# Performance work log

Measured on AMD Instinct MI355X. Metric: run time of the kernel, lower is better.

Reference implementation:

```python
import jax, jax.numpy as jnp
import numpy as np

EPS_BN = 1e-5
EPS_LN = 1e-5

def _bn(x, g, b, m, v):
    # inference-mode BatchNorm2d over channel dim 1
    scale = g / jnp.sqrt(v + EPS_BN)
    return x * scale[None, :, None, None] + (b - m * scale)[None, :, None, None]

def _conv1x1(x, w, b=None):
    y = jnp.einsum('bchw,oc->bohw', x, w)
    if b is not None:
        y = y + b[None, :, None, None]
    return y

def _gelu(x):
    return jax.nn.gelu(x, approximate=False)

def setup_inputs() -> dict:
    key = jax.random.key(0)
    ks = jax.random.split(key, 40)
    B, C, H, W = 32, 160, 56, 56
    C5, C3 = C // 5, C * 3
    s = 0.05
    d = {}
    d['x'] = jax.random.normal(ks[0], (B, C, H, W), jnp.float32)
    d['bn1_g'] = jax.random.uniform(ks[1], (C,), jnp.float32, 0.5, 1.5)
    d['bn1_b'] = jax.random.normal(ks[2], (C,)) * s
    d['bn1_m'] = jax.random.normal(ks[3], (C,)) * s
    d['bn1_v'] = jnp.ones((C,), jnp.float32)
    names = ['t', 'b', 'r', 'l', 'c']
    for i, n in enumerate(names):
        d['w' + n] = jax.random.normal(ks[4 + i], (C5, C)) * s
        d['b' + n] = jax.random.normal(ks[9 + i], (C5,)) * s
    d['wf1'] = jax.random.normal(ks[14], (C, C)) * s
    d['bf1'] = jax.random.normal(ks[15], (C,)) * s
    d['bn2_g'] = jax.random.uniform(ks[16], (C,), jnp.float32, 0.5, 1.5)
    d['bn2_b'] = jax.random.normal(ks[17], (C,)) * s
    d['bn2_m'] = jax.random.normal(ks[18], (C,)) * s
    d['bn2_v'] = jnp.ones((C,), jnp.float32)
    d['wph'] = jax.random.normal(ks[19], (W, W)) * s
    d['bph'] = jax.random.normal(ks[20], (W,)) * s
    d['wpw'] = jax.random.normal(ks[21], (H, H)) * s
    d['bpw'] = jax.random.normal(ks[22], (H,)) * s
    d['wf2'] = jax.random.normal(ks[23], (C, C3)) * s
    d['ln_g'] = jax.random.uniform(ks[24], (C,), jnp.float32, 0.5, 1.5)
    d['ln_b'] = jax.random.normal(ks[25], (C,)) * s
    d['wfc1'] = jax.random.normal(ks[26], (C3, C)) * s
    d['bfc1'] = jax.random.normal(ks[27], (C3,)) * s
    d['wfc2'] = jax.random.normal(ks[28], (C, C3)) * s
    d['bfc2'] = jax.random.normal(ks[29], (C,)) * s
    d['step'] = 1
    return d

def reference(x, bn1_g, bn1_b, bn1_m, bn1_v, wt, bt, wb, bb, wr, br, wl, bl, wc, bc,
              wf1, bf1, bn2_g, bn2_b, bn2_m, bn2_v, wph, bph, wpw, bpw, wf2,
              ln_g, ln_b, wfc1, bfc1, wfc2, bfc2, step):
    B, C, H, W = x.shape
    # ---- localMix: ShiftedPillarsConcatentation_BNAct_NP5 ----
    h = _gelu(_bn(x, bn1_g, bn1_b, bn1_m, bn1_v))
    x_t = _conv1x1(h, wt, bt)
    x_b = _conv1x1(h, wb, bb)
    x_r = _conv1x1(h, wr, br)
    x_l = _conv1x1(h, wl, bl)
    x_c = _conv1x1(h, wc, bc)
    # pad then narrow exactly as torch: t/l shift by 1, b/r shift by step
    x_t = jnp.pad(x_t, ((0, 0), (0, 0), (0, step), (0, 0)))[:, :, 1:1 + H, :]
    x_b = jnp.pad(x_b, ((0, 0), (0, 0), (step, 0), (0, 0)))[:, :, 0:H, :]
    x_l = jnp.pad(x_l, ((0, 0), (0, 0), (0, 0), (0, step)))[:, :, :, 1:1 + W]
    x_r = jnp.pad(x_r, ((0, 0), (0, 0), (0, 0), (step, 0)))[:, :, :, 0:W]
    lm = _conv1x1(jnp.concatenate([x_t, x_b, x_r, x_l, x_c], axis=1), wf1, bf1)
    # ---- globalMix: sparseMLP_BNAct ----
    g = _gelu(_bn(lm, bn2_g, bn2_b, bn2_m, bn2_v))
    # proj_h mixes the W axis (input permuted to (B,W,C,H)), bias per output W
    x_h = jnp.einsum('bchw,vw->bchv', g, wph) + bph[None, None, None, :]
    # proj_w mixes the H axis (input permuted to (B,H,C,W)), bias per output H
    x_w = jnp.einsum('bchw,uh->bcuw', g, wpw) + bpw[None, None, :, None]
    gm = _conv1x1(jnp.concatenate([g, x_h, x_w], axis=1), wf2)  # no bias
    x1 = gm + x  # residual 1
    # ---- channelMix: LN + Mlp over channels ----
    y = jnp.transpose(x1, (0, 2, 3, 1))  # BHWC
    mu = jnp.mean(y, axis=-1, keepdims=True)
    var = jnp.mean(jnp.square(y - mu), axis=-1, keepdims=True)
    y = (y - mu) / jnp.sqrt(var + EPS_LN) * ln_g + ln_b
    y = _gelu(jnp.einsum('bhwc,fc->bhwf', y, wfc1) + bfc1)
    y = jnp.einsum('bhwf,cf->bhwc', y, wfc2) + bfc2
    return jnp.transpose(y, (0, 3, 1, 2)) + x1  # residual 2
```

## Files before the change

kernel.cpp:

```cpp
#include <hip/hip_runtime.h>
#include <hip/hip_bf16.h>
#include <math.h>

typedef __hip_bfloat16 bf16;
typedef __attribute__((ext_vector_type(8))) short s8v;
typedef __attribute__((ext_vector_type(4))) float f4v;
typedef __attribute__((ext_vector_type(4))) unsigned short u4v;

#define Bn  32
#define Cn  160
#define HWn 3136
#define Pn  100352

__device__ __forceinline__ float b2f(bf16 v){ return __bfloat162float(v); }
__device__ __forceinline__ bf16  f2b(float v){ return __float2bfloat16(v); }
__device__ __forceinline__ float bits2f(unsigned short u){
    union { float f; unsigned int i; } x; x.i = ((unsigned int)u) << 16; return x.f;
}
__device__ __forceinline__ unsigned short f2bits(float v){
    union { unsigned short us; bf16 b; } cv; cv.b = f2b(v); return cv.us;
}
__device__ __forceinline__ float gelu_f(float x){
    float ax = fabsf(x) * 0.7071067811865476f;
    float t  = 1.0f / (1.0f + 0.3275911f*ax);
    float p  = ((((1.061405429f*t - 1.453152027f)*t + 1.421413741f)*t
                 - 0.284496736f)*t + 0.254829592f)*t;
    float e  = __expf(-ax*ax);
    float erfv = 1.0f - p*e;
    float s = (x >= 0.f) ? erfv : -erfv;
    return 0.5f*x*(1.0f + s);
}

#define MFMA(a,b,c) __builtin_amdgcn_mfma_f32_16x16x32_bf16((a),(b),(c),0,0,0)

__global__ __launch_bounds__(256) void k0_prep(
    const float* __restrict__ wt, const float* __restrict__ wb_, const float* __restrict__ wr,
    const float* __restrict__ wl, const float* __restrict__ wc,
    const float* __restrict__ bt, const float* __restrict__ bb_, const float* __restrict__ br,
    const float* __restrict__ bl, const float* __restrict__ bc,
    const float* __restrict__ wf1, const float* __restrict__ bf1,
    const float* __restrict__ g2, const float* __restrict__ b2, const float* __restrict__ m2, const float* __restrict__ v2,
    const float* __restrict__ wf2, const float* __restrict__ wfc1, const float* __restrict__ wfc2,
    const float* __restrict__ wph, const float* __restrict__ wpw,
    const float* __restrict__ lng, const float* __restrict__ lnb, const float* __restrict__ bfc1,
    bf16* wcat, bf16* wf1b, bf16* wf2b, bf16* wfc1g, bf16* wfc2b, bf16* wphb, bf16* wpwb,
    float* bcat, float* epsv, float* eptv, float* wgs, float* wcb)
{
    int idx = blockIdx.x*256 + threadIdx.x;
    if (idx < 25600){ int o = idx/160, k = idx - o*160; int gi = o>>5, oo = o&31;
        const float* wp = gi==0?wt: gi==1?wb_: gi==2?wr: gi==3?wl: wc;
        wcat[idx] = f2b(wp[oo*160+k]); return; }
    idx -= 25600;
    if (idx < 25600){ wf1b[idx] = f2b(wf1[idx]); return; }
    idx -= 25600;
    if (idx < 76800){ wf2b[idx] = f2b(wf2[idx]); return; }
    idx -= 76800;
    if (idx < 76800){ int f = idx/160, c = idx - f*160;
        wfc1g[idx] = f2b(wfc1[f*160+c] * lng[c]); return; }
    idx -= 76800;
    if (idx < 76800){ wfc2b[idx] = f2b(wfc2[idx]); return; }
    idx -= 76800;
    if (idx < 4096){ int v = idx>>6, w = idx&63;
        wphb[idx] = (v<56 && w<56) ? f2b(wph[v*56+w]) : f2b(0.f); return; }
    idx -= 4096;
    if (idx < 4096){ int v = idx>>6, w = idx&63;
        wpwb[idx] = (v<56 && w<56) ? f2b(wpw[v*56+w]) : f2b(0.f); return; }
    idx -= 4096;
    if (idx < 160){ int o = idx; int gi = o>>5, oo = o&31;
        const float* bp = gi==0?bt: gi==1?bb_: gi==2?br: gi==3?bl: bc;
        bcat[o] = bp[oo]; return; }
    idx -= 160;
    if (idx < 160){ int o = idx; float s = g2[o]*rsqrtf(v2[o]+1e-5f);
        epsv[o] = s; eptv[o] = (bf1[o]-m2[o])*s + b2[o]; return; }
    idx -= 160;
    if (idx < 480){ int o = idx; float sg = 0.f, sb = 0.f;
        const float* wr_ = wfc1 + (size_t)o*160;
        for (int c = 0; c < 160; ++c){ float w = wr_[c]; sg += w*lng[c]; sb += w*lnb[c]; }
        wgs[o] = sg; wcb[o] = sb + bfc1[o]; return; }
}

__global__ __launch_bounds__(256) void k12_bn_conv5(const float* __restrict__ x,
    const float* __restrict__ g, const float* __restrict__ b,
    const float* __restrict__ m_, const float* __restrict__ v,
    const bf16* __restrict__ wcat, const float* __restrict__ bcat, bf16* __restrict__ y5T)
{
    __shared__ __align__(16) unsigned short Bs[2][16*168];
    __shared__ __align__(16) char AsB[64*320];
    __shared__ float sc[160], sh[160];
    int tid = threadIdx.x, wave = tid>>6, lane = tid&63, m = lane&15, q = lane>>4;
    int blk = blockIdx.x; int bb = blk/49; int hw0 = (blk - bb*49)*64;
    if (tid < 160){
        float s = g[tid] * rsqrtf(v[tid] + 1e-5f);
        sc[tid] = s; sh[tid] = b[tid] - m_[tid]*s;
    }
    { const s8v* sp = (const s8v*)((const unsigned short*)wcat);
      for (int c = tid; c < 320; c += 256){ int row = c/20, col = (c - row*20)*8;
          *(s8v*)&Bs[0][row*168 + col] = sp[c]; } }
    __syncthreads();
    const float* xb = x + (size_t)bb*Cn*HWn + hw0;
    for (int idx = tid; idx < 160*64; idx += 256){
        int c = idx >> 6, p = idx & 63;
        float val = xb[(size_t)c*HWn + p];
        unsigned short us = f2bits(gelu_f(val*sc[c] + sh[c]));
        int off = (p*320 + c*2) ^ ((p&7)<<4);
        *(unsigned short*)(AsB + off) = us;
    }
    __syncthreads();
    size_t pos0 = (size_t)bb*HWn + hw0;
    s8v a[5];
    {
        int row = wave*16 + m; int xr = (row&7)<<4;
        #pragma unroll
        for (int kb = 0; kb < 5; ++kb){
            int off = (row*320 + (q*8 + kb*32)*2) ^ xr;
            a[kb] = *(const s8v*)(AsB + off);
        }
    }
    for (int s = 0; s < 10; ++s){
        if (s+1 < 10){
            const s8v* sp = (const s8v*)((const unsigned short*)wcat + (size_t)(s+1)*2560);
            for (int c = tid; c < 320; c += 256){ int row = c/20, col = (c - row*20)*8;
                *(s8v*)&Bs[(s+1)&1][row*168 + col] = sp[c]; }
        }
        f4v acc = {0.f,0.f,0.f,0.f};
        const unsigned short* Bp = &Bs[s&1][m*168 + q*8];
        #pragma unroll
        for (int kb = 0; kb < 5; ++kb) acc = MFMA(a[kb], *(const s8v*)(Bp + kb*32), acc);
        float bias = bcat[s*16 + m];
        bf16* yo = y5T + (pos0 + wave*16 + q*4)*160 + s*16 + m;
        #pragma unroll
        for (int r = 0; r < 4; ++r) yo[r*160] = f2b(acc[r] + bias);
        __syncthreads();
    }
}

__global__ __launch_bounds__(256) void k3_wf1(const bf16* __restrict__ y5T,
    const bf16* __restrict__ wf1b, const float* __restrict__ epsv, const float* __restrict__ eptv,
    bf16* __restrict__ gT)
{
    __shared__ __align__(16) unsigned short Bs[2][16*168];
    int tid = threadIdx.x, wave = tid>>6, lane = tid&63, m = lane&15, q = lane>>4;
    int blk = blockIdx.x; int bb = blk/49; int hw0 = (blk - bb*49)*64;
    size_t pos0 = (size_t)bb*HWn + hw0;
    int phw = hw0 + wave*16 + m; int h = phw/56, w = phw - h*56;
    s8v a[5];
    #pragma unroll
    for (int kb = 0; kb < 5; ++kb){
        int h2 = h, w2 = w; bool ok = true;
        if      (kb == 0){ h2 = h+1; ok = (h2 < 56); }
        else if (kb == 1){ h2 = h-1; ok = (h2 >= 0); }
        else if (kb == 2){ w2 = w-1; ok = (w2 >= 0); }
        else if (kb == 3){ w2 = w+1; ok = (w2 < 56); }
        if (ok){
            const unsigned short* Ap = (const unsigned short*)y5T +
                ((size_t)bb*HWn + h2*56 + w2)*160 + kb*32 + q*8;
            a[kb] = *(const s8v*)Ap;
        } else {
            a[kb] = (s8v){0,0,0,0,0,0,0,0};
        }
    }
    { const s8v* sp = (const s8v*)((const unsigned short*)wf1b);
      for (int c = tid; c < 320; c += 256){ int row = c/20, col = (c - row*20)*8;
          *(s8v*)&Bs[0][row*168 + col] = sp[c]; } }
    __syncthreads();
    for (int s = 0; s < 10; ++s){
        if (s+1 < 10){
            const s8v* sp = (const s8v*)((const unsigned short*)wf1b + (size_t)(s+1)*2560);
            for (int c = tid; c < 320; c += 256){ int row = c/20, col = (c - row*20)*8;
                *(s8v*)&Bs[(s+1)&1][row*168 + col] = sp[c]; }
        }
        f4v acc = {0.f,0.f,0.f,0.f};
        const unsigned short* Bp = &Bs[s&1][m*168 + q*8];
        #pragma unroll
        for (int kb = 0; kb < 5; ++kb) acc = MFMA(a[kb], *(const s8v*)(Bp + kb*32), acc);
        int o = s*16 + m;
        float es = epsv[o], et = eptv[o];
        bf16* go = gT + (pos0 + wave*16 + q*4)*160 + o;
        #pragma unroll
        for (int r = 0; r < 4; ++r) go[r*160] = f2b(gelu_f(acc[r]*es + et));
        __syncthreads();
    }
}

__global__ __launch_bounds__(256) void k4_projh(const bf16* __restrict__ gT,
    const bf16* __restrict__ wphb, const float* __restrict__ bph, bf16* __restrict__ xhT)
{
    __shared__ __align__(16) unsigned short gS[160*72];
    int tid = threadIdx.x, wave = tid>>6, lane = tid&63, m = lane&15, q = lane>>4;
    int blk = blockIdx.x; int b = blk/56, h = blk - b*56;
    const unsigned short* ga = (const unsigned short*)gT + ((size_t)b*HWn + h*56)*160;
    for (int idx = tid; idx < 56*160; idx += 256){
        int w = idx/160, c = idx - w*160;
        gS[c*72 + w] = ga[idx];
    }
    for (int idx = tid; idx < 160*8; idx += 256){
        int c = idx>>3, w = 56 + (idx&7);
        gS[c*72 + w] = 0;
    }
    __syncthreads();
    int v0 = wave*16;
    s8v a[2];
    #pragma unroll
    for (int kb = 0; kb < 2; ++kb)
        a[kb] = *(const s8v*)((const unsigned short*)wphb + (v0+m)*64 + kb*32 + q*8);
    int v = v0 + q*4;
    for (int s = 0; s < 10; ++s){
        f4v acc = {0.f,0.f,0.f,0.f};
        const unsigned short* Bp = &gS[(s*16+m)*72 + q*8];
        #pragma unroll
        for (int kb = 0; kb < 2; ++kb) acc = MFMA(a[kb], *(const s8v*)(Bp + kb*32), acc);
        #pragma unroll
        for (int r = 0; r < 4; ++r){
            int vv = v + r;
            if (vv < 56)
                xhT[((size_t)b*HWn + h*56 + vv)*160 + s*16 + m] = f2b(acc[r] + bph[vv]);
        }
    }
}

__global__ __launch_bounds__(256) void k5_projw(const bf16* __restrict__ gT,
    const bf16* __restrict__ wpwb, const float* __restrict__ bpw, bf16* __restrict__ xwT)
{
    __shared__ __align__(16) unsigned short gS[160*72];
    int tid = threadIdx.x, wave = tid>>6, lane = tid&63, m = lane&15, q = lane>>4;
    int blk = blockIdx.x; int b = blk/56, w = blk - b*56;
    const unsigned short* gbase = (const unsigned short*)gT + ((size_t)b*HWn + w)*160;
    for (int idx = tid; idx < 56*160; idx += 256){
        int hh = idx/160, c = idx - hh*160;
        gS[c*72 + hh] = gbase[(size_t)hh*56*160 + c];
    }
    for (int idx = tid; idx < 160*8; idx += 256){
        int c = idx>>3, hh = 56 + (idx&7);
        gS[c*72 + hh] = 0;
    }
    __syncthreads();
    int v0 = wave*16;
    s8v a[2];
    #pragma unroll
    for (int kb = 0; kb < 2; ++kb)
        a[kb] = *(const s8v*)((const unsigned short*)wpwb + (v0+m)*64 + kb*32 + q*8);
    int v = v0 + q*4;
    for (int s = 0; s < 10; ++s){
        f4v acc = {0.f,0.f,0.f,0.f};
        const unsigned short* Bp = &gS[(s*16+m)*72 + q*8];
        #pragma unroll
        for (int kb = 0; kb < 2; ++kb) acc = MFMA(a[kb], *(const s8v*)(Bp + kb*32), acc);
        #pragma unroll
        for (int r = 0; r < 4; ++r){
            int vv = v + r;
            if (vv < 56)
                xwT[((size_t)b*HWn + vv*56 + w)*160 + s*16 + m] = f2b(acc[r] + bpw[vv]);
        }
    }
}

__global__ __launch_bounds__(256) void k6_wf2(const bf16* __restrict__ gT,
    const bf16* __restrict__ xhT, const bf16* __restrict__ xwT,
    const bf16* __restrict__ wf2b, bf16* __restrict__ gm)
{
    __shared__ __align__(16) unsigned short Bs[2][16*488];
    int tid = threadIdx.x, wave = tid>>6, lane = tid&63, m = lane&15, q = lane>>4;
    size_t pos0 = (size_t)blockIdx.x*64;
    size_t prow = (pos0 + wave*16 + m)*160;
    s8v a[15];
    #pragma unroll
    for (int kb = 0; kb < 15; ++kb){
        const bf16* src = (kb < 5) ? gT : (kb < 10 ? xhT : xwT);
        int kc = (kb - (kb < 5 ? 0 : (kb < 10 ? 5 : 10)))*32 + q*8;
        a[kb] = *(const s8v*)((const unsigned short*)src + prow + kc);
    }
    { const s8v* sp = (const s8v*)((const unsigned short*)wf2b);
      for (int c = tid; c < 960; c += 256){ int row = c/60, col = (c - row*60)*8;
          *(s8v*)&Bs[0][row*488 + col] = sp[c]; } }
    __syncthreads();
    for (int s = 0; s < 10; ++s){
        if (s+1 < 10){
            const s8v* sp = (const s8v*)((const unsigned short*)wf2b + (size_t)(s+1)*7680);
            for (int c = tid; c < 960; c += 256){ int row = c/60, col = (c - row*60)*8;
                *(s8v*)&Bs[(s+1)&1][row*488 + col] = sp[c]; }
        }
        f4v acc = {0.f,0.f,0.f,0.f};
        const unsigned short* Bp = &Bs[s&1][m*488 + q*8];
        #pragma unroll
        for (int kb = 0; kb < 15; ++kb) acc = MFMA(a[kb], *(const s8v*)(Bp + kb*32), acc);
        bf16* go = gm + (pos0 + wave*16 + q*4)*160 + s*16 + m;
        #pragma unroll
        for (int r = 0; r < 4; ++r) go[r*160] = f2b(acc[r]);
        __syncthreads();
    }
}

__global__ __launch_bounds__(256,3) void k78_mlp(const float* __restrict__ x,
    const bf16* __restrict__ gm,
    const bf16* __restrict__ wfc1g, const float* __restrict__ wcb,
    const bf16* __restrict__ wfc2b, const float* __restrict__ bfc2,
    float* __restrict__ out)
{
    __shared__ __align__(16) char lds[51200];
    float* Xs = (float*)lds;
    char* UsB = lds;
    char* AsB = lds + 30720;
    char* GsB = lds + 40960;

    int tid = threadIdx.x, wave = tid>>6, lane = tid&63, m = lane&15, q = lane>>4;
    int rt = wave&1, chh = wave>>1;
    int blk = blockIdx.x; int bb = blk/98; int hw0 = (blk - bb*98)*32;
    size_t pos0 = (size_t)bb*HWn + hw0;
    const float* xb = x + (size_t)bb*Cn*HWn + hw0;

    for (int idx = tid; idx < 160*32; idx += 256){
        int c = idx >> 5, p = idx & 31;
        Xs[p*164 + c] = xb[(size_t)c*HWn + p];
    }
    __syncthreads();

    {
        int p = tid >> 3, q8 = tid & 7; int c0 = q8*20;
        const unsigned short* gp = (const unsigned short*)gm + (pos0 + p)*160 + c0;
        float y[20]; float s = 0.f, ss = 0.f;
        #pragma unroll
        for (int j = 0; j < 5; ++j){
            u4v gv = *(const u4v*)(gp + j*4);
            *(u4v*)(GsB + p*320 + (c0 + j*4)*2) = gv;
            f4v xv = *(const f4v*)&Xs[p*164 + c0 + j*4];
            #pragma unroll
            for (int t = 0; t < 4; ++t){
                float vv = xv[t] + bits2f(gv[t]);
                y[j*4 + t] = vv; s += vv; ss += vv*vv;
            }
        }
        s += __shfl_xor(s, 1); ss += __shfl_xor(ss, 1);
        s += __shfl_xor(s, 2); ss += __shfl_xor(ss, 2);
        s += __shfl_xor(s, 4); ss += __shfl_xor(ss, 4);
        float mean = s * (1.f/160.f);
        float var  = ss * (1.f/160.f) - mean*mean;
        float rstd = rsqrtf(var + 1e-5f);
        int xr = (p&7)<<4;
        #pragma unroll
        for (int j = 0; j < 5; ++j){
            u4v pk;
            #pragma unroll
            for (int t = 0; t < 4; ++t) pk[t] = f2bits((y[j*4 + t] - mean)*rstd);
            int off = (p*320 + (c0 + j*4)*2) ^ xr;
            *(u4v*)(AsB + off) = pk;
        }
    }
    __syncthreads();

    {
        s8v a1[5];
        {
            int row = rt*16 + m; int xr = (row&7)<<4;
            #pragma unroll
            for (int kb = 0; kb < 5; ++kb){
                int off = (row*320 + (q*8 + kb*32)*2) ^ xr;
                a1[kb] = *(const s8v*)(AsB + off);
            }
        }
        const unsigned short* W1 = (const unsigned short*)wfc1g + ((size_t)chh*15*16 + m)*160 + q*8;
        s8v b0[5], b1[5];
        #pragma unroll
        for (int kb = 0; kb < 5; ++kb) b0[kb] = *(const s8v*)(W1 + kb*32);
        #pragma unroll
        for (int s = 0; s < 15; ++s){
            if (s + 1 < 15){
                const unsigned short* Wn = W1 + (size_t)(s+1)*2560;
                #pragma unroll
                for (int kb = 0; kb < 5; ++kb) b1[kb] = *(const s8v*)(Wn + kb*32);
            }
            f4v acc = {0.f,0.f,0.f,0.f};
            #pragma unroll
            for (int kb = 0; kb < 5; ++kb) acc = MFMA(a1[kb], b0[kb], acc);
            int o = (chh*15 + s)*16 + m;
            float wc = wcb[o];
            #pragma unroll
            for (int r = 0; r < 4; ++r){
                int row = rt*16 + q*4 + r;
                int off = (row*960 + o*2) ^ ((row&7)<<4);
                *(unsigned short*)(UsB + off) = f2bits(gelu_f(acc[r] + wc));
            }
            if (s + 1 < 15){
                #pragma unroll
                for (int kb = 0; kb < 5; ++kb) b0[kb] = b1[kb];
            }
        }
    }
    __syncthreads();

    {
        s8v a2[15];
        {
            int row = rt*16 + m; int xr = (row&7)<<4;
            #pragma unroll
            for (int kb = 0; kb < 15; ++kb){
                int off = (row*960 + (q*8 + kb*32)*2) ^ xr;
                a2[kb] = *(const s8v*)(UsB + off);
            }
        }
        #pragma unroll
        for (int s = 0; s < 5; ++s){
            int o = chh*80 + s*16 + m;
            const unsigned short* W2 = (const unsigned short*)wfc2b + (size_t)o*480 + q*8;
            s8v b2[15];
            #pragma unroll
            for (int kb = 0; kb < 15; ++kb) b2[kb] = *(const s8v*)(W2 + kb*32);
            f4v acc = {0.f,0.f,0.f,0.f};
            #pragma unroll
            for (int kb = 0; kb < 15; ++kb) acc = MFMA(a2[kb], b2[kb], acc);
            float bias = bfc2[o];
            const float* xp = x + (size_t)bb*Cn*HWn + (size_t)o*HWn + hw0 + rt*16 + q*4;
            f4v x4 = *(const f4v*)xp;
            f4v o4;
            #pragma unroll
            for (int r = 0; r < 4; ++r){
                int row = rt*16 + q*4 + r;
                float gmv = bits2f(*(const unsigned short*)(GsB + row*320 + o*2));
                o4[r] = x4[r] + gmv + acc[r] + bias;
            }
            float* op = out + (size_t)bb*Cn*HWn + (size_t)o*HWn + hw0 + rt*16 + q*4;
            *(f4v*)op = o4;
        }
    }
}

extern "C" void kernel_launch(void* const* d_in, const int* in_sizes, int n_in,
                              void* d_out, int out_size, void* d_ws, size_t ws_size,
                              hipStream_t stream)
{
    (void)in_sizes; (void)n_in; (void)out_size; (void)ws_size;
    const float* x     = (const float*)d_in[0];
    const float* bn1g  = (const float*)d_in[1];
    const float* bn1b  = (const float*)d_in[2];
    const float* bn1m  = (const float*)d_in[3];
    const float* bn1v  = (const float*)d_in[4];
    const float* wt    = (const float*)d_in[5];
    const float* bt    = (const float*)d_in[6];
    const float* wb    = (const float*)d_in[7];
    const float* bb    = (const float*)d_in[8];
    const float* wr    = (const float*)d_in[9];
    const float* br    = (const float*)d_in[10];
    const float* wl    = (const float*)d_in[11];
    const float* bl    = (const float*)d_in[12];
    const float* wc    = (const float*)d_in[13];
    const float* bc    = (const float*)d_in[14];
    const float* wf1   = (const float*)d_in[15];
    const float* bf1   = (const float*)d_in[16];
    const float* bn2g  = (const float*)d_in[17];
    const float* bn2b  = (const float*)d_in[18];
    const float* bn2m  = (const float*)d_in[19];
    const float* bn2v  = (const float*)d_in[20];
    const float* wph   = (const float*)d_in[21];
    const float* bph   = (const float*)d_in[22];
    const float* wpw   = (const float*)d_in[23];
    const float* bpw   = (const float*)d_in[24];
    const float* wf2   = (const float*)d_in[25];
    const float* lng   = (const float*)d_in[26];
    const float* lnb   = (const float*)d_in[27];
    const float* wfc1  = (const float*)d_in[28];
    const float* bfc1  = (const float*)d_in[29];
    const float* wfc2  = (const float*)d_in[30];
    const float* bfc2v = (const float*)d_in[31];
    float* outp = (float*)d_out;

    const size_t PC2 = (size_t)Pn*160*2;
    char* ws = (char*)d_ws;
    bf16* y5T  = (bf16*)(ws + 1*PC2);
    bf16* gT   = (bf16*)(ws + 2*PC2);
    bf16* xhT  = (bf16*)(ws + 3*PC2);
    bf16* xwT  = (bf16*)(ws + 4*PC2);
    bf16* gm   = (bf16*)(ws + 5*PC2);
    char* wsw  = ws + 6*PC2;
    bf16*  wcat  = (bf16*)(wsw + 0);
    bf16*  wf1b  = (bf16*)(wsw + 51200);
    bf16*  wf2b  = (bf16*)(wsw + 102400);
    bf16*  wfc1g = (bf16*)(wsw + 256000);
    bf16*  wfc2b = (bf16*)(wsw + 409600);
    bf16*  wphb  = (bf16*)(wsw + 563200);
    bf16*  wpwb  = (bf16*)(wsw + 571392);
    float* bcat  = (float*)(wsw + 579584);
    float* epsv  = (float*)(wsw + 580224);
    float* eptv  = (float*)(wsw + 580864);
    float* wgs   = (float*)(wsw + 581504);
    float* wcb   = (float*)(wsw + 583424);

    const int GP = Pn/64;
    const int GS = Bn*56;
    const int GF = Pn/32;

    k0_prep<<<1136, 256, 0, stream>>>(wt, wb, wr, wl, wc, bt, bb, br, bl, bc,
                                      wf1, bf1, bn2g, bn2b, bn2m, bn2v,
                                      wf2, wfc1, wfc2, wph, wpw,
                                      lng, lnb, bfc1,
                                      wcat, wf1b, wf2b, wfc1g, wfc2b, wphb, wpwb,
                                      bcat, epsv, eptv, wgs, wcb);
    k12_bn_conv5 <<<GP, 256, 0, stream>>>(x, bn1g, bn1b, bn1m, bn1v, wcat, bcat, y5T);
    k3_wf1       <<<GP, 256, 0, stream>>>(y5T, wf1b, epsv, eptv, gT);
    k4_projh     <<<GS, 256, 0, stream>>>(gT, wphb, bph, xhT);
    k5_projw     <<<GS, 256, 0, stream>>>(gT, wpwb, bpw, xwT);
    k6_wf2       <<<GP, 256, 0, stream>>>(gT, xhT, xwT, wf2b, gm);
    k78_mlp      <<<GF, 256, 0, stream>>>(x, gm, wfc1g, wcb, wfc2b, bfc2v, outp);
}
```

Before: 482.9 us.

## Fuse wf2 projection GEMM into channel-MLP kernel, dropping gm round-trip

Removes the separate k6_wf2 kernel and computes the 480->160 wf2 projection inside the MLP kernel, writing results straight into shared memory instead of a global gm buffer. Each wave computes a 16-row by 80-channel slice, loading the wf2 weights directly from global memory (L2) into registers rather than staging them in LDS. This saves a launch and a full write-and-read of the bf16 activation tensor. In exchange the MLP kernel gets more register pressure (30 s8v vectors) under its 3-block occupancy bound, and it re-reads the weights once per 32-position tile.

Result: slower. 501.1 us (+3.8%).

```diff
diff --git a/kernel.cpp b/kernel.cpp
--- a/kernel.cpp
+++ b/kernel.cpp
@@ -254,44 +254,9 @@
     }
 }
 
-__global__ __launch_bounds__(256) void k6_wf2(const bf16* __restrict__ gT,
-    const bf16* __restrict__ xhT, const bf16* __restrict__ xwT,
-    const bf16* __restrict__ wf2b, bf16* __restrict__ gm)
-{
-    __shared__ __align__(16) unsigned short Bs[2][16*488];
-    int tid = threadIdx.x, wave = tid>>6, lane = tid&63, m = lane&15, q = lane>>4;
-    size_t pos0 = (size_t)blockIdx.x*64;
-    size_t prow = (pos0 + wave*16 + m)*160;
-    s8v a[15];
-    #pragma unroll
-    for (int kb = 0; kb < 15; ++kb){
-        const bf16* src = (kb < 5) ? gT : (kb < 10 ? xhT : xwT);
-        int kc = (kb - (kb < 5 ? 0 : (kb < 10 ? 5 : 10)))*32 + q*8;
-        a[kb] = *(const s8v*)((const unsigned short*)src + prow + kc);
-    }
-    { const s8v* sp = (const s8v*)((const unsigned short*)wf2b);
-      for (int c = tid; c < 960; c += 256){ int row = c/60, col = (c - row*60)*8;
-          *(s8v*)&Bs[0][row*488 + col] = sp[c]; } }
-    __syncthreads();
-    for (int s = 0; s < 10; ++s){
-        if (s+1 < 10){
-            const s8v* sp = (const s8v*)((const unsigned short*)wf2b + (size_t)(s+1)*7680);
-            for (int c = tid; c < 960; c += 256){ int row = c/60, col = (c - row*60)*8;
-                *(s8v*)&Bs[(s+1)&1][row*488 + col] = sp[c]; }
-        }
-        f4v acc = {0.f,0.f,0.f,0.f};
-        const unsigned short* Bp = &Bs[s&1][m*488 + q*8];
-        #pragma unroll
-        for (int kb = 0; kb < 15; ++kb) acc = MFMA(a[kb], *(const s8v*)(Bp + kb*32), acc);
-        bf16* go = gm + (pos0 + wave*16 + q*4)*160 + s*16 + m;
-        #pragma unroll
-        for (int r = 0; r < 4; ++r) go[r*160] = f2b(acc[r]);
-        __syncthreads();
-    }
-}
-
-__global__ __launch_bounds__(256,3) void k78_mlp(const float* __restrict__ x,
-    const bf16* __restrict__ gm,
+__global__ __launch_bounds__(256,3) void k678_mlp(const float* __restrict__ x,
+    const bf16* __restrict__ gT, const bf16* __restrict__ xhT, const bf16* __restrict__ xwT,
+    const bf16* __restrict__ wf2b,
     const bf16* __restrict__ wfc1g, const float* __restrict__ wcb,
     const bf16* __restrict__ wfc2b, const float* __restrict__ bfc2,
     float* __restrict__ out)
@@ -312,16 +277,38 @@
         int c = idx >> 5, p = idx & 31;
         Xs[p*164 + c] = xb[(size_t)c*HWn + p];
     }
+
+    {
+        s8v a0[15];
+        #pragma unroll
+        for (int kb = 0; kb < 15; ++kb){
+            const bf16* src = (kb < 5) ? gT : (kb < 10 ? xhT : xwT);
+            int kc = (kb - (kb < 5 ? 0 : (kb < 10 ? 5 : 10)))*32 + q*8;
+            a0[kb] = *(const s8v*)((const unsigned short*)src + (pos0 + rt*16 + m)*160 + kc);
+        }
+        #pragma unroll
+        for (int s = 0; s < 5; ++s){
+            int o = chh*80 + s*16 + m;
+            const unsigned short* W2 = (const unsigned short*)wf2b + (size_t)o*480 + q*8;
+            s8v bw[15];
+            #pragma unroll
+            for (int kb = 0; kb < 15; ++kb) bw[kb] = *(const s8v*)(W2 + kb*32);
+            f4v acc = {0.f,0.f,0.f,0.f};
+            #pragma unroll
+            for (int kb = 0; kb < 15; ++kb) acc = MFMA(a0[kb], bw[kb], acc);
+            #pragma unroll
+            for (int r = 0; r < 4; ++r)
+                *(unsigned short*)(GsB + (rt*16 + q*4 + r)*320 + o*2) = f2bits(acc[r]);
+        }
+    }
     __syncthreads();
 
     {
         int p = tid >> 3, q8 = tid & 7; int c0 = q8*20;
-        const unsigned short* gp = (const unsigned short*)gm + (pos0 + p)*160 + c0;
         float y[20]; float s = 0.f, ss = 0.f;
         #pragma unroll
         for (int j = 0; j < 5; ++j){
-            u4v gv = *(const u4v*)(gp + j*4);
-            *(u4v*)(GsB + p*320 + (c0 + j*4)*2) = gv;
+            u4v gv = *(const u4v*)(GsB + p*320 + (c0 + j*4)*2);
             f4v xv = *(const f4v*)&Xs[p*164 + c0 + j*4];
             #pragma unroll
             for (int t = 0; t < 4; ++t){
@@ -468,7 +455,6 @@
     bf16* gT   = (bf16*)(ws + 2*PC2);
     bf16* xhT  = (bf16*)(ws + 3*PC2);
     bf16* xwT  = (bf16*)(ws + 4*PC2);
-    bf16* gm   = (bf16*)(ws + 5*PC2);
     char* wsw  = ws + 6*PC2;
     bf16*  wcat  = (bf16*)(wsw + 0);
     bf16*  wf1b  = (bf16*)(wsw + 51200);
@@ -497,6 +483,6 @@
     k3_wf1       <<<GP, 256, 0, stream>>>(y5T, wf1b, epsv, eptv, gT);
     k4_projh     <<<GS, 256, 0, stream>>>(gT, wphb, bph, xhT);
     k5_projw     <<<GS, 256, 0, stream>>>(gT, wpwb, bpw, xwT);
-    k6_wf2       <<<GP, 256, 0, stream>>>(gT, xhT, xwT, wf2b, gm);
-    k78_mlp      <<<GF, 256, 0, stream>>>(x, gm, wfc1g, wcb, wfc2b, bfc2v, outp);
-}
+    k678_mlp     <<<GF, 256, 0, stream>>>(x, gT, xhT, xwT, wf2b,
+                                          wfc1g, wcb, wfc2b, bfc2v, outp);
+}
```
